# Optimization experiments

Measured on AMD Instinct MI355X. Metric: run time of the kernel, lower is better.

Reference implementation:

```python
import jax, jax.numpy as jnp
import numpy as np

B, H, W, C = 8, 128, 128, 128
SCALE = C ** -0.5
EPS = 1e-6  # flax LayerNorm default


def layer_norm(x, scale, bias):
    m = jnp.mean(x, axis=-1, keepdims=True)
    v = jnp.var(x, axis=-1, keepdims=True)
    return (x - m) * jax.lax.rsqrt(v + EPS) * scale + bias


def setup_inputs() -> dict:
    key = jax.random.key(0)
    ks = jax.random.split(key, 12)
    std = 0.02
    return {
        "x_l": jax.random.normal(ks[0], (B, H, W, C), jnp.float32),
        "x_r": jax.random.normal(ks[1], (B, H, W, C), jnp.float32),
        "ln_l_scale": jnp.ones((C,), jnp.float32),
        "ln_l_bias": jnp.zeros((C,), jnp.float32),
        "ln_r_scale": jnp.ones((C,), jnp.float32),
        "ln_r_bias": jnp.zeros((C,), jnp.float32),
        "w_ql": jax.random.normal(ks[2], (C, C), jnp.float32) * std,
        "b_ql": jnp.zeros((C,), jnp.float32),
        "w_qr": jax.random.normal(ks[3], (C, C), jnp.float32) * std,
        "b_qr": jnp.zeros((C,), jnp.float32),
        "w_vl": jax.random.normal(ks[4], (C, C), jnp.float32) * std,
        "b_vl": jnp.zeros((C,), jnp.float32),
        "w_vr": jax.random.normal(ks[5], (C, C), jnp.float32) * std,
        "b_vr": jnp.zeros((C,), jnp.float32),
        "beta": jax.random.normal(ks[6], (1, 1, 1, C), jnp.float32) * std,
        "gamma": jax.random.normal(ks[7], (1, 1, 1, C), jnp.float32) * std,
    }


def reference(x_l, x_r, ln_l_scale, ln_l_bias, ln_r_scale, ln_r_bias,
              w_ql, b_ql, w_qr, b_qr, w_vl, b_vl, w_vr, b_vr, beta, gamma):
    # Q projections of layer-normed inputs  [B,H,W,C]
    q_l = layer_norm(x_l, ln_l_scale, ln_l_bias) @ w_ql + b_ql
    q_r = layer_norm(x_r, ln_r_scale, ln_r_bias) @ w_qr + b_qr
    # V projections of raw inputs
    v_l = x_l @ w_vl + b_vl
    v_r = x_r @ w_vr + b_vr
    # shared cross-view score matrix over the width axis: [B,H,W_l,W_r]
    attention = jnp.einsum('bhic,bhjc->bhij', q_l, q_r) * SCALE
    # dual softmax: rows (axis=-1) and transposed columns
    f_r2l = jnp.einsum('bhij,bhjc->bhic', jax.nn.softmax(attention, axis=-1), v_r) * beta
    f_l2r = jnp.einsum('bhji,bhjc->bhic',
                       jax.nn.softmax(attention, axis=-2), v_l) * gamma
    return (x_l + f_r2l, x_r + f_l2r)
```

## Files before the change

kernel.cpp:

```cpp
#include <hip/hip_runtime.h>


typedef __attribute__((ext_vector_type(8))) __bf16 bf16x8;
typedef __attribute__((ext_vector_type(4))) __bf16 bf16x4;
typedef __attribute__((ext_vector_type(4))) float f4;

#define MFMA(A, B, C) __builtin_amdgcn_mfma_f32_16x16x32_bf16((A), (B), (C), 0, 0, 0)
#define SCALE_QK 0.08838834764831845f

static __device__ __forceinline__ int eoff(int n, int k) {
  return (n << 8) + ((((k >> 3) ^ (n & 7)) << 4) | ((k & 7) << 1));
}

__global__ void prep_w(const float* __restrict__ w0, const float* __restrict__ w1,
                       const float* __restrict__ w2, const float* __restrict__ w3,
                       __bf16* __restrict__ out) {
  int m = blockIdx.y;
  const float* src = (m == 0) ? w0 : (m == 1) ? w1 : (m == 2) ? w2 : w3;
  int t = blockIdx.x * 256 + threadIdx.x;
  int k = t >> 7, n = t & 127;
  out[m * 16384 + n * 128 + k] = (__bf16)src[k * 128 + n];
}

static __device__ __forceinline__ void ln_frags(const float* __restrict__ xp, size_t base,
                                                const float* __restrict__ g,
                                                const float* __restrict__ b, int row,
                                                int quad, bf16x8* lF) {
  float4 v[8];
#pragma unroll
  for (int t = 0; t < 8; ++t)
    v[t] = *(const float4*)(xp + base + row * 128 + (t >> 1) * 32 + quad * 8 + (t & 1) * 4);
  float s = 0.f, s2 = 0.f;
#pragma unroll
  for (int t = 0; t < 8; ++t) {
    s += v[t].x + v[t].y + v[t].z + v[t].w;
    s2 += v[t].x * v[t].x + v[t].y * v[t].y + v[t].z * v[t].z + v[t].w * v[t].w;
  }
  s += __shfl_xor(s, 16);
  s += __shfl_xor(s, 32);
  s2 += __shfl_xor(s2, 16);
  s2 += __shfl_xor(s2, 32);
  float mean = s * 0.0078125f;
  float var = s2 * 0.0078125f - mean * mean;
  float rstd = rsqrtf(var + 1e-6f);
#pragma unroll
  for (int ks = 0; ks < 4; ++ks) {
    bf16x8 lu;
#pragma unroll
    for (int t = 0; t < 2; ++t) {
      float4 q = v[ks * 2 + t];
      float4 gv = *(const float4*)(g + ks * 32 + quad * 8 + t * 4);
      float4 bv = *(const float4*)(b + ks * 32 + quad * 8 + t * 4);
      lu[t * 4 + 0] = (__bf16)((q.x - mean) * rstd * gv.x + bv.x);
      lu[t * 4 + 1] = (__bf16)((q.y - mean) * rstd * gv.y + bv.y);
      lu[t * 4 + 2] = (__bf16)((q.z - mean) * rstd * gv.z + bv.z);
      lu[t * 4 + 3] = (__bf16)((q.w - mean) * rstd * gv.w + bv.w);
    }
    lF[ks] = lu;
  }
}

static __device__ __forceinline__ void x_frags(const float* __restrict__ xp, size_t base,
                                               int row, int quad, bf16x8* xF) {
#pragma unroll
  for (int ks = 0; ks < 4; ++ks) {
    bf16x8 xu;
#pragma unroll
    for (int t = 0; t < 2; ++t) {
      float4 q = *(const float4*)(xp + base + row * 128 + ks * 32 + quad * 8 + t * 4);
      xu[t * 4 + 0] = (__bf16)q.x;
      xu[t * 4 + 1] = (__bf16)q.y;
      xu[t * 4 + 2] = (__bf16)q.z;
      xu[t * 4 + 3] = (__bf16)q.w;
    }
    xF[ks] = xu;
  }
}

template <int TRANSPOSED>
static __device__ __forceinline__ void proj_g(const bf16x8* aF,
                                              const __bf16* __restrict__ wTm, char* dst,
                                              const float* __restrict__ bias, float scale,
                                              int w, int l16, int quad) {
#pragma unroll 2
  for (int nt = 0; nt < 8; ++nt) {
    f4 a = {0.f, 0.f, 0.f, 0.f};
    const __bf16* wrow = wTm + (nt * 16 + l16) * 128 + quad * 8;
#pragma unroll
    for (int ks = 0; ks < 4; ++ks) {
      bf16x8 bf = *(const bf16x8*)(wrow + ks * 32);
      a = MFMA(aF[ks], bf, a);
    }
    float bs = bias[nt * 16 + l16];
    if (TRANSPOSED) {
      int c = nt * 16 + l16;
      bf16x4 u;
#pragma unroll
      for (int r = 0; r < 4; ++r) u[r] = (__bf16)((a[r] + bs) * scale);
      *(bf16x4*)(dst + eoff(c, w * 16 + quad * 4)) = u;
    } else {
#pragma unroll
      for (int r = 0; r < 4; ++r) {
        int i = w * 16 + quad * 4 + r;
        *(__bf16*)(dst + eoff(i, nt * 16 + l16)) = (__bf16)((a[r] + bs) * scale);
      }
    }
  }
}

static __device__ __forceinline__ void pv_epi(const bf16x8* pF, const char* vslot,
                                              const float* __restrict__ xp, size_t base,
                                              const float* __restrict__ scl,
                                              float* __restrict__ outp, int w, int l16,
                                              int quad) {
#pragma unroll 2
  for (int nt = 0; nt < 8; ++nt) {
    f4 a = {0.f, 0.f, 0.f, 0.f};
#pragma unroll
    for (int ks = 0; ks < 4; ++ks) {
      bf16x8 bf = *(const bf16x8*)(vslot + eoff(nt * 16 + l16, ks * 32 + quad * 8));
      a = MFMA(pF[ks], bf, a);
    }
    int c = nt * 16 + l16;
    float sv = scl[c];
#pragma unroll
    for (int r = 0; r < 4; ++r) {
      int i = w * 16 + quad * 4 + r;
      outp[base + i * 128 + c] = xp[base + i * 128 + c] + sv * (float)a[r];
    }
  }
}

__global__ __launch_bounds__(512, 4) void scam_fused(
    const float* __restrict__ xl, const float* __restrict__ xr,
    const float* __restrict__ gl, const float* __restrict__ bl,
    const float* __restrict__ gr, const float* __restrict__ br,
    const __bf16* __restrict__ wT,
    const float* __restrict__ bql, const float* __restrict__ bqr,
    const float* __restrict__ bvl, const float* __restrict__ bvr,
    const float* __restrict__ beta, const float* __restrict__ gamma,
    float* __restrict__ out0, float* __restrict__ out1) {
  __shared__ char S[73728];
  char* S1 = S;
  char* S2 = S + 32768;
  float* colred0 = (float*)(S + 65536);
  float* colred1 = (float*)(S + 69632);
  int tid = threadIdx.x;
  int lane = tid & 63, w = tid >> 6;
  int quad = lane >> 4, l16 = lane & 15;
  int row = w * 16 + l16;
  size_t base = (size_t)blockIdx.x << 14;

  {
    bf16x8 llF[4];
    ln_frags(xl, base, gl, bl, row, quad, llF);
    proj_g<0>(llF, wT, S1, bql, SCALE_QK, w, l16, quad);
  }
  {
    bf16x8 lrF[4];
    ln_frags(xr, base, gr, br, row, quad, lrF);
    proj_g<0>(lrF, wT + 16384, S2, bqr, 1.0f, w, l16, quad);
  }
  __syncthreads();

  bf16x8 qlF[4];
#pragma unroll
  for (int ks = 0; ks < 4; ++ks)
    qlF[ks] = *(const bf16x8*)(S1 + eoff(row, ks * 32 + quad * 8));

  f4 sacc[8];
#pragma unroll
  for (int nt = 0; nt < 8; ++nt) {
    f4 z = {0.f, 0.f, 0.f, 0.f};
    sacc[nt] = z;
  }
#pragma unroll
  for (int nt = 0; nt < 8; ++nt)
#pragma unroll
    for (int ks = 0; ks < 4; ++ks) {
      bf16x8 bf = *(const bf16x8*)(S2 + eoff(nt * 16 + l16, ks * 32 + quad * 8));
      sacc[nt] = MFMA(qlF[ks], bf, sacc[nt]);
    }

  float rm[4], rinv[4];
#pragma unroll
  for (int r = 0; r < 4; ++r) {
    float m = -1e30f;
#pragma unroll
    for (int nt = 0; nt < 8; ++nt) m = fmaxf(m, sacc[nt][r]);
#pragma unroll
    for (int d = 1; d < 16; d <<= 1) m = fmaxf(m, __shfl_xor(m, d));
    float s = 0.f;
#pragma unroll
    for (int nt = 0; nt < 8; ++nt) s += __expf(sacc[nt][r] - m);
#pragma unroll
    for (int d = 1; d < 16; d <<= 1) s += __shfl_xor(s, d);
    rm[r] = m;
    rinv[r] = 1.f / s;
  }
  float cm[8], cinv[8];
#pragma unroll
  for (int nt = 0; nt < 8; ++nt) {
    float m = fmaxf(fmaxf(sacc[nt][0], sacc[nt][1]), fmaxf(sacc[nt][2], sacc[nt][3]));
    m = fmaxf(m, __shfl_xor(m, 16));
    m = fmaxf(m, __shfl_xor(m, 32));
    cm[nt] = m;
  }
  if (quad == 0) {
#pragma unroll
    for (int nt = 0; nt < 8; ++nt) colred0[w * 128 + nt * 16 + l16] = cm[nt];
  }
  __syncthreads();
#pragma unroll
  for (int nt = 0; nt < 8; ++nt) {
    float m = cm[nt];
#pragma unroll
    for (int ww = 0; ww < 8; ++ww) m = fmaxf(m, colred0[ww * 128 + nt * 16 + l16]);
    cm[nt] = m;
  }
#pragma unroll
  for (int nt = 0; nt < 8; ++nt) {
    float s = __expf(sacc[nt][0] - cm[nt]) + __expf(sacc[nt][1] - cm[nt]) +
              __expf(sacc[nt][2] - cm[nt]) + __expf(sacc[nt][3] - cm[nt]);
    s += __shfl_xor(s, 16);
    s += __shfl_xor(s, 32);
    cinv[nt] = s;
  }
  if (quad == 0) {
#pragma unroll
    for (int nt = 0; nt < 8; ++nt) colred1[w * 128 + nt * 16 + l16] = cinv[nt];
  }
  __syncthreads();
#pragma unroll
  for (int nt = 0; nt < 8; ++nt) {
    float s = 0.f;
#pragma unroll
    for (int ww = 0; ww < 8; ++ww) s += colred1[ww * 128 + nt * 16 + l16];
    cinv[nt] = 1.f / s;
  }

#pragma unroll
  for (int nt = 0; nt < 8; ++nt) {
    bf16x4 pc;
#pragma unroll
    for (int r = 0; r < 4; ++r) {
      float sv = sacc[nt][r];
      int i = w * 16 + quad * 4 + r;
      *(__bf16*)(S1 + eoff(i, nt * 16 + l16)) = (__bf16)(__expf(sv - rm[r]) * rinv[r]);
      pc[r] = (__bf16)(__expf(sv - cm[nt]) * cinv[nt]);
    }
    *(bf16x4*)(S2 + eoff(nt * 16 + l16, w * 16 + quad * 4)) = pc;
  }

  bf16x8 xrF[4];
  x_frags(xr, base, row, quad, xrF);
  __syncthreads();

  bf16x8 prF[4], pcF[4];
#pragma unroll
  for (int ks = 0; ks < 4; ++ks) {
    prF[ks] = *(const bf16x8*)(S1 + eoff(row, ks * 32 + quad * 8));
    pcF[ks] = *(const bf16x8*)(S2 + eoff(row, ks * 32 + quad * 8));
  }
  __syncthreads();

  proj_g<1>(xrF, wT + 3 * 16384, S1, bvr, 1.0f, w, l16, quad);
  {
    bf16x8 xlF[4];
    x_frags(xl, base, row, quad, xlF);
    proj_g<1>(xlF, wT + 2 * 16384, S2, bvl, 1.0f, w, l16, quad);
  }
  __syncthreads();

  pv_epi(prF, S1, xl, base, beta, out0, w, l16, quad);
  pv_epi(pcF, S2, xr, base, gamma, out1, w, l16, quad);
}

extern "C" void kernel_launch(void* const* d_in, const int* in_sizes, int n_in,
                              void* d_out, int out_size, void* d_ws, size_t ws_size,
                              hipStream_t stream) {
  const float* xl = (const float*)d_in[0];
  const float* xr = (const float*)d_in[1];
  const float* gl = (const float*)d_in[2];
  const float* bl = (const float*)d_in[3];
  const float* gr = (const float*)d_in[4];
  const float* br = (const float*)d_in[5];
  const float* wql = (const float*)d_in[6];
  const float* bql = (const float*)d_in[7];
  const float* wqr = (const float*)d_in[8];
  const float* bqr = (const float*)d_in[9];
  const float* wvl = (const float*)d_in[10];
  const float* bvl = (const float*)d_in[11];
  const float* wvr = (const float*)d_in[12];
  const float* bvr = (const float*)d_in[13];
  const float* beta = (const float*)d_in[14];
  const float* gamma = (const float*)d_in[15];

  __bf16* wT = (__bf16*)d_ws;
  float* out0 = (float*)d_out;
  float* out1 = out0 + (size_t)8 * 128 * 128 * 128;

  prep_w<<<dim3(64, 4), 256, 0, stream>>>(wql, wqr, wvl, wvr, wT);
  scam_fused<<<1024, 512, 0, stream>>>(xl, xr, gl, bl, gr, br, wT, bql, bqr, bvl, bvr,
                                       beta, gamma, out0, out1);
}
```

Measured before the change: 390.1 us.

## Merge column max/sum reduction into one barrier and reorder PV stages

Computes the per-wave column max and sum together and combines them across waves with an online-softmax rescale, replacing two block barriers with one. It writes the row-softmax probabilities earlier and issues the x_r load sooner so the global-load latency overlaps the column reduction. The two value projections and PV epilogues are interleaved sequentially, which lowers live register pressure but adds a barrier in the tail and costs extra exp evaluations in the cross-wave combine.

After: 386.3 us. About the same (-1.0%).

```diff
diff --git a/kernel.cpp b/kernel.cpp
--- a/kernel.cpp
+++ b/kernel.cpp
@@ -182,60 +182,69 @@
       sacc[nt] = MFMA(qlF[ks], bf, sacc[nt]);
     }
 
-  float rm[4], rinv[4];
-#pragma unroll
-  for (int r = 0; r < 4; ++r) {
-    float m = -1e30f;
-#pragma unroll
-    for (int nt = 0; nt < 8; ++nt) m = fmaxf(m, sacc[nt][r]);
-#pragma unroll
-    for (int d = 1; d < 16; d <<= 1) m = fmaxf(m, __shfl_xor(m, d));
-    float s = 0.f;
-#pragma unroll
-    for (int nt = 0; nt < 8; ++nt) s += __expf(sacc[nt][r] - m);
-#pragma unroll
-    for (int d = 1; d < 16; d <<= 1) s += __shfl_xor(s, d);
-    rm[r] = m;
-    rinv[r] = 1.f / s;
-  }
+  {
+    float rm[4], rinv[4];
+#pragma unroll
+    for (int r = 0; r < 4; ++r) {
+      float m = -1e30f;
+#pragma unroll
+      for (int nt = 0; nt < 8; ++nt) m = fmaxf(m, sacc[nt][r]);
+#pragma unroll
+      for (int d = 1; d < 16; d <<= 1) m = fmaxf(m, __shfl_xor(m, d));
+      float s = 0.f;
+#pragma unroll
+      for (int nt = 0; nt < 8; ++nt) s += __expf(sacc[nt][r] - m);
+#pragma unroll
+      for (int d = 1; d < 16; d <<= 1) s += __shfl_xor(s, d);
+      rm[r] = m;
+      rinv[r] = 1.f / s;
+    }
+#pragma unroll
+    for (int nt = 0; nt < 8; ++nt) {
+#pragma unroll
+      for (int r = 0; r < 4; ++r) {
+        int i = w * 16 + quad * 4 + r;
+        *(__bf16*)(S1 + eoff(i, nt * 16 + l16)) =
+            (__bf16)(__expf(sacc[nt][r] - rm[r]) * rinv[r]);
+      }
+    }
+  }
+
+  bf16x8 xrF[4];
+  x_frags(xr, base, row, quad, xrF);
+
   float cm[8], cinv[8];
 #pragma unroll
   for (int nt = 0; nt < 8; ++nt) {
     float m = fmaxf(fmaxf(sacc[nt][0], sacc[nt][1]), fmaxf(sacc[nt][2], sacc[nt][3]));
     m = fmaxf(m, __shfl_xor(m, 16));
     m = fmaxf(m, __shfl_xor(m, 32));
-    cm[nt] = m;
-  }
-  if (quad == 0) {
-#pragma unroll
-    for (int nt = 0; nt < 8; ++nt) colred0[w * 128 + nt * 16 + l16] = cm[nt];
-  }
-  __syncthreads();
-#pragma unroll
-  for (int nt = 0; nt < 8; ++nt) {
-    float m = cm[nt];
-#pragma unroll
-    for (int ww = 0; ww < 8; ++ww) m = fmaxf(m, colred0[ww * 128 + nt * 16 + l16]);
-    cm[nt] = m;
-  }
-#pragma unroll
-  for (int nt = 0; nt < 8; ++nt) {
-    float s = __expf(sacc[nt][0] - cm[nt]) + __expf(sacc[nt][1] - cm[nt]) +
-              __expf(sacc[nt][2] - cm[nt]) + __expf(sacc[nt][3] - cm[nt]);
+    float s = __expf(sacc[nt][0] - m) + __expf(sacc[nt][1] - m) +
+              __expf(sacc[nt][2] - m) + __expf(sacc[nt][3] - m);
     s += __shfl_xor(s, 16);
     s += __shfl_xor(s, 32);
+    cm[nt] = m;
     cinv[nt] = s;
   }
   if (quad == 0) {
 #pragma unroll
-    for (int nt = 0; nt < 8; ++nt) colred1[w * 128 + nt * 16 + l16] = cinv[nt];
-  }
-  __syncthreads();
-#pragma unroll
-  for (int nt = 0; nt < 8; ++nt) {
+    for (int nt = 0; nt < 8; ++nt) {
+      colred0[w * 128 + nt * 16 + l16] = cm[nt];
+      colred1[w * 128 + nt * 16 + l16] = cinv[nt];
+    }
+  }
+  __syncthreads();
+#pragma unroll
+  for (int nt = 0; nt < 8; ++nt) {
+    float m = -1e30f;
+#pragma unroll
+    for (int ww = 0; ww < 8; ++ww) m = fmaxf(m, colred0[ww * 128 + nt * 16 + l16]);
     float s = 0.f;
 #pragma unroll
-    for (int ww = 0; ww < 8; ++ww) s += colred1[ww * 128 + nt * 16 + l16];
+    for (int ww = 0; ww < 8; ++ww)
+      s += colred1[ww * 128 + nt * 16 + l16] *
+           __expf(colred0[ww * 128 + nt * 16 + l16] - m);
+    cm[nt] = m;
     cinv[nt] = 1.f / s;
   }
 
@@ -243,36 +252,33 @@
   for (int nt = 0; nt < 8; ++nt) {
     bf16x4 pc;
 #pragma unroll
-    for (int r = 0; r < 4; ++r) {
-      float sv = sacc[nt][r];
-      int i = w * 16 + quad * 4 + r;
-      *(__bf16*)(S1 + eoff(i, nt * 16 + l16)) = (__bf16)(__expf(sv - rm[r]) * rinv[r]);
-      pc[r] = (__bf16)(__expf(sv - cm[nt]) * cinv[nt]);
-    }
+    for (int r = 0; r < 4; ++r)
+      pc[r] = (__bf16)(__expf(sacc[nt][r] - cm[nt]) * cinv[nt]);
     *(bf16x4*)(S2 + eoff(nt * 16 + l16, w * 16 + quad * 4)) = pc;
   }
 
-  bf16x8 xrF[4];
-  x_frags(xr, base, row, quad, xrF);
-  __syncthreads();
-
-  bf16x8 prF[4], pcF[4];
-#pragma unroll
-  for (int ks = 0; ks < 4; ++ks) {
+  bf16x8 prF[4];
+#pragma unroll
+  for (int ks = 0; ks < 4; ++ks)
     prF[ks] = *(const bf16x8*)(S1 + eoff(row, ks * 32 + quad * 8));
+  __syncthreads();
+
+  proj_g<1>(xrF, wT + 3 * 16384, S1, bvr, 1.0f, w, l16, quad);
+  bf16x8 xlF[4];
+  x_frags(xl, base, row, quad, xlF);
+  __syncthreads();
+
+  pv_epi(prF, S1, xl, base, beta, out0, w, l16, quad);
+
+  bf16x8 pcF[4];
+#pragma unroll
+  for (int ks = 0; ks < 4; ++ks)
     pcF[ks] = *(const bf16x8*)(S2 + eoff(row, ks * 32 + quad * 8));
-  }
-  __syncthreads();
-
-  proj_g<1>(xrF, wT + 3 * 16384, S1, bvr, 1.0f, w, l16, quad);
-  {
-    bf16x8 xlF[4];
-    x_frags(xl, base, row, quad, xlF);
-    proj_g<1>(xlF, wT + 2 * 16384, S2, bvl, 1.0f, w, l16, quad);
-  }
-  __syncthreads();
-
-  pv_epi(prF, S1, xl, base, beta, out0, w, l16, quad);
+  __syncthreads();
+
+  proj_g<1>(xlF, wT + 2 * 16384, S2, bvl, 1.0f, w, l16, quad);
+  __syncthreads();
+
   pv_epi(pcF, S2, xr, base, gamma, out1, w, l16, quad);
 }
 
```
